# Performance work log

Hardware: AMD Instinct MI355X
Metric: run time of the kernel (lower is better)

## Reference

```python
import jax, jax.numpy as jnp
import numpy as np

# dims from QBN_GRU_Base.__init__ with in_dim=64
IN_DIM = 64
OBS_MID = 28   # int(abs(64 - 8) / 2)
OBS_BN = 8
M_SIZE = 16
LATENT = 16
M_BN = 8
T, B = 512, 2048


def _lin_params(key, out_d, in_d):
    # normc init: normal(0,1) rows scaled to unit L2 norm, zero bias
    w = jax.random.normal(key, (out_d, in_d), dtype=jnp.float32)
    w = w / jnp.sqrt(jnp.sum(w * w, axis=1, keepdims=True))
    b = jnp.zeros((out_d,), dtype=jnp.float32)
    return w, b


def setup_inputs() -> dict:
    key = jax.random.key(0)
    ks = jax.random.split(key, 16)
    x = jax.random.normal(ks[0], (T, B, IN_DIM), dtype=jnp.float32)
    obs_w0, obs_b0 = _lin_params(ks[1], OBS_MID, IN_DIM)
    obs_w1, obs_b1 = _lin_params(ks[2], OBS_MID, OBS_MID)
    obs_w2, obs_b2 = _lin_params(ks[3], OBS_BN, OBS_MID)
    s = float(1.0 / np.sqrt(M_SIZE))  # torch GRUCell default init
    gru_wih = jax.random.uniform(ks[4], (3 * M_SIZE, OBS_BN), jnp.float32, -s, s)
    gru_whh = jax.random.uniform(ks[5], (3 * M_SIZE, M_SIZE), jnp.float32, -s, s)
    gru_bih = jax.random.uniform(ks[6], (3 * M_SIZE,), jnp.float32, -s, s)
    gru_bhh = jax.random.uniform(ks[7], (3 * M_SIZE,), jnp.float32, -s, s)
    m2q_w0, m2q_b0 = _lin_params(ks[8], LATENT, M_SIZE)
    m2q_w1, m2q_b1 = _lin_params(ks[9], LATENT, LATENT)
    m2q_w2, m2q_b2 = _lin_params(ks[10], M_BN, LATENT)
    q2m_w0, q2m_b0 = _lin_params(ks[11], LATENT, M_BN)
    q2m_w1, q2m_b1 = _lin_params(ks[12], LATENT, LATENT)
    q2m_w2, q2m_b2 = _lin_params(ks[13], M_SIZE, LATENT)
    act_w, act_b = _lin_params(ks[14], LATENT, M_SIZE)
    return dict(x=x,
                obs_w0=obs_w0, obs_b0=obs_b0, obs_w1=obs_w1, obs_b1=obs_b1,
                obs_w2=obs_w2, obs_b2=obs_b2,
                gru_wih=gru_wih, gru_whh=gru_whh, gru_bih=gru_bih, gru_bhh=gru_bhh,
                m2q_w0=m2q_w0, m2q_b0=m2q_b0, m2q_w1=m2q_w1, m2q_b1=m2q_b1,
                m2q_w2=m2q_w2, m2q_b2=m2q_b2,
                q2m_w0=q2m_w0, q2m_b0=q2m_b0, q2m_w1=q2m_w1, q2m_b1=q2m_b1,
                q2m_w2=q2m_w2, q2m_b2=q2m_b2,
                act_w=act_w, act_b=act_b)


def _ternary_tanh(v):
    # QBN soft ternary activation with straight-through rounding to {-1,0,1}
    soft = 1.5 * jnp.tanh(v) + 0.5 * jnp.tanh(-3.0 * v)
    return soft + jax.lax.stop_gradient(jnp.round(soft) - soft)


def reference(x, obs_w0, obs_b0, obs_w1, obs_b1, obs_w2, obs_b2,
              gru_wih, gru_whh, gru_bih, gru_bhh,
              m2q_w0, m2q_b0, m2q_w1, m2q_b1, m2q_w2, m2q_b2,
              q2m_w0, q2m_b0, q2m_w1, q2m_b1, q2m_w2, q2m_b2,
              act_w, act_b):
    # observation QBN encoder, applied to all timesteps at once [T,B,in]->[T,B,8]
    h = jnp.tanh(x @ obs_w0.T + obs_b0)
    h = jnp.tanh(h @ obs_w1.T + obs_b1)
    xq = _ternary_tanh(h @ obs_w2.T + obs_b2)

    def step(hid, x_t):
        # torch.nn.GRUCell math
        gi = x_t @ gru_wih.T + gru_bih        # [B, 3*M]
        gh = hid @ gru_whh.T + gru_bhh
        ir, iz, inn = jnp.split(gi, 3, axis=-1)
        hr, hz, hn = jnp.split(gh, 3, axis=-1)
        r = jax.nn.sigmoid(ir + hr)
        z = jax.nn.sigmoid(iz + hz)
        n = jnp.tanh(inn + r * hn)
        ht = (1.0 - z) * n + z * hid
        # memory -> quantized bottleneck
        q = jnp.tanh(ht @ m2q_w0.T + m2q_b0)
        q = jnp.tanh(q @ m2q_w1.T + m2q_b1)
        q = _ternary_tanh(q @ m2q_w2.T + m2q_b2)
        # bottleneck -> memory (all layers tanh)
        m = jnp.tanh(q @ q2m_w0.T + q2m_b0)
        m = jnp.tanh(m @ q2m_w1.T + q2m_b1)
        m = jnp.tanh(m @ q2m_w2.T + q2m_b2)
        return m, m  # new hidden, and per-step output y

    h0 = jnp.zeros((x.shape[1], M_SIZE), dtype=x.dtype)
    _, ys = jax.lax.scan(step, h0, xq)        # [T, B, M_SIZE]
    return jnp.tanh(ys @ act_w.T + act_b)     # action latent [T, B, LATENT]
```

## Files before the change

### kernel.cpp

```cpp
#include <hip/hip_runtime.h>


#define T_DIM 512
#define B_DIM 2048
#define NELEM (T_DIM * B_DIM)

__device__ __forceinline__ float tanh_xla(float x) {
  const float kClamp = 7.99881172180175781f;
  float xc = fminf(fmaxf(x, -kClamp), kClamp);
  float x2 = xc * xc;
  float p = fmaf(x2, -2.76076847742355e-16f, 2.00018790482477e-13f);
  p = fmaf(x2, p, -8.60467152213735e-11f);
  p = fmaf(x2, p, 5.12229709037114e-08f);
  p = fmaf(x2, p, 1.48572235717979e-05f);
  p = fmaf(x2, p, 6.37261928875436e-04f);
  p = fmaf(x2, p, 4.89352455891786e-03f);
  p = xc * p;
  float q = fmaf(x2, 1.19825839466702e-06f, 1.18534705686654e-04f);
  q = fmaf(x2, q, 2.26843463243900e-03f);
  q = fmaf(x2, q, 4.89352518554385e-03f);
  float r = p / q;
  return (fabsf(x) < 0.0004f) ? x : r;
}

__device__ __forceinline__ float sigmoid_xla(float x) {
  return 0.5f + 0.5f * tanh_xla(0.5f * x);
}

__device__ __forceinline__ int ternary_digit(float v) {
  float soft = 1.5f * tanh_xla(v) + 0.5f * tanh_xla(-3.0f * v);
  return (int)rintf(soft) + 1;
}

__global__ __launch_bounds__(256) void k_obs(
    const float* __restrict__ x,
    const float* __restrict__ w0, const float* __restrict__ b0,
    const float* __restrict__ w1, const float* __restrict__ b1,
    const float* __restrict__ w2, const float* __restrict__ b2,
    unsigned short* __restrict__ xcodes) {
  int e = blockIdx.x * 256 + threadIdx.x;
  const float* xr = x + (size_t)e * 64;
  float xv[64];
#pragma unroll
  for (int j = 0; j < 64; j += 4) {
    float4 v = *reinterpret_cast<const float4*>(xr + j);
    xv[j] = v.x; xv[j + 1] = v.y; xv[j + 2] = v.z; xv[j + 3] = v.w;
  }
  float h1[28];
#pragma unroll
  for (int k = 0; k < 28; ++k) {
    float acc = 0.0f;
#pragma unroll
    for (int j = 0; j < 64; ++j) acc = fmaf(w0[k * 64 + j], xv[j], acc);
    h1[k] = tanh_xla(acc + b0[k]);
  }
  float h2[28];
#pragma unroll
  for (int k = 0; k < 28; ++k) {
    float acc = 0.0f;
#pragma unroll
    for (int j = 0; j < 28; ++j) acc = fmaf(w1[k * 28 + j], h1[j], acc);
    h2[k] = tanh_xla(acc + b1[k]);
  }
  const int p3[8] = {1, 3, 9, 27, 81, 243, 729, 2187};
  unsigned code = 0;
#pragma unroll
  for (int k = 0; k < 8; ++k) {
    float acc = 0.0f;
#pragma unroll
    for (int j = 0; j < 28; ++j) acc = fmaf(w2[k * 28 + j], h2[j], acc);
    code += (unsigned)(ternary_digit(acc + b2[k]) * p3[k]);
  }
  xcodes[e] = (unsigned short)code;
}

__global__ __launch_bounds__(256) void k_gi(
    const float* __restrict__ wih, const float* __restrict__ bih,
    float* __restrict__ gip) {
  int c = blockIdx.x * 256 + threadIdx.x;
  if (c >= 6561) return;
  float q[8];
  unsigned cc = (unsigned)c;
#pragma unroll
  for (int k = 0; k < 8; ++k) { q[k] = (float)((int)(cc % 3u) - 1); cc /= 3u; }
#pragma unroll
  for (int i = 0; i < 16; ++i) {
    float gr = 0.f, gz = 0.f, gn = 0.f;
#pragma unroll
    for (int j = 0; j < 8; ++j) {
      gr = fmaf(wih[i * 8 + j], q[j], gr);
      gz = fmaf(wih[(16 + i) * 8 + j], q[j], gz);
      gn = fmaf(wih[(32 + i) * 8 + j], q[j], gn);
    }
    float4 o;
    o.x = gr + bih[i]; o.y = gz + bih[16 + i]; o.z = gn + bih[32 + i]; o.w = 0.f;
    *reinterpret_cast<float4*>(gip + (size_t)c * 64 + i * 4) = o;
  }
}

__global__ __launch_bounds__(256) void k_mtab(
    const float* __restrict__ q2m_w0, const float* __restrict__ q2m_b0,
    const float* __restrict__ q2m_w1, const float* __restrict__ q2m_b1,
    const float* __restrict__ q2m_w2, const float* __restrict__ q2m_b2,
    const float* __restrict__ whh, const float* __restrict__ bhh,
    const float* __restrict__ act_w, const float* __restrict__ act_b,
    float* __restrict__ ghm, float* __restrict__ ytab) {
  int c = blockIdx.x * 256 + threadIdx.x;
  if (c > 6561) return;
  float m[16];
  if (c == 6561) {
#pragma unroll
    for (int i = 0; i < 16; ++i) m[i] = 0.0f;
  } else {
    float q[8];
    unsigned cc = (unsigned)c;
#pragma unroll
    for (int k = 0; k < 8; ++k) { q[k] = (float)((int)(cc % 3u) - 1); cc /= 3u; }
    float a[16];
#pragma unroll
    for (int i = 0; i < 16; ++i) {
      float acc = 0.f;
#pragma unroll
      for (int j = 0; j < 8; ++j) acc = fmaf(q2m_w0[i * 8 + j], q[j], acc);
      a[i] = tanh_xla(acc + q2m_b0[i]);
    }
    float d[16];
#pragma unroll
    for (int i = 0; i < 16; ++i) {
      float acc = 0.f;
#pragma unroll
      for (int j = 0; j < 16; ++j) acc = fmaf(q2m_w1[i * 16 + j], a[j], acc);
      d[i] = tanh_xla(acc + q2m_b1[i]);
    }
#pragma unroll
    for (int i = 0; i < 16; ++i) {
      float acc = 0.f;
#pragma unroll
      for (int j = 0; j < 16; ++j) acc = fmaf(q2m_w2[i * 16 + j], d[j], acc);
      m[i] = tanh_xla(acc + q2m_b2[i]);
    }
  }
#pragma unroll
  for (int i = 0; i < 16; ++i) {
    float gr = 0.f, gz = 0.f, gn = 0.f;
#pragma unroll
    for (int j = 0; j < 16; ++j) {
      gr = fmaf(whh[i * 16 + j], m[j], gr);
      gz = fmaf(whh[(16 + i) * 16 + j], m[j], gz);
      gn = fmaf(whh[(32 + i) * 16 + j], m[j], gn);
    }
    float4 o;
    o.x = gr + bhh[i]; o.y = gz + bhh[16 + i]; o.z = gn + bhh[32 + i]; o.w = m[i];
    *reinterpret_cast<float4*>(ghm + (size_t)c * 64 + i * 4) = o;
  }
  if (c < 6561) {
#pragma unroll
    for (int i = 0; i < 16; ++i) {
      float acc = 0.f;
#pragma unroll
      for (int j = 0; j < 16; ++j) acc = fmaf(act_w[i * 16 + j], m[j], acc);
      ytab[(size_t)c * 16 + i] = tanh_xla(acc + act_b[i]);
    }
  }
}

__global__ __launch_bounds__(64) void k_scan(
    const unsigned short* __restrict__ xcodes,
    const float* __restrict__ ghm,
    const float* __restrict__ gip,
    const float* __restrict__ m2q_w0, const float* __restrict__ m2q_b0,
    const float* __restrict__ m2q_w1, const float* __restrict__ m2q_b1,
    const float* __restrict__ m2q_w2, const float* __restrict__ m2q_b2,
    unsigned short* __restrict__ qcodes) {
  int lane = threadIdx.x & 15;
  int b = (blockIdx.x * 64 + threadIdx.x) >> 4;
  float w0r[16], w1r[16], w2r[16];
#pragma unroll
  for (int j = 0; j < 16; j += 4) {
    float4 a = *reinterpret_cast<const float4*>(m2q_w0 + lane * 16 + j);
    w0r[j] = a.x; w0r[j + 1] = a.y; w0r[j + 2] = a.z; w0r[j + 3] = a.w;
    float4 bq = *reinterpret_cast<const float4*>(m2q_w1 + lane * 16 + j);
    w1r[j] = bq.x; w1r[j + 1] = bq.y; w1r[j + 2] = bq.z; w1r[j + 3] = bq.w;
    float4 cq = *reinterpret_cast<const float4*>(m2q_w2 + (lane & 7) * 16 + j);
    w2r[j] = cq.x; w2r[j + 1] = cq.y; w2r[j + 2] = cq.z; w2r[j + 3] = cq.w;
  }
  float b0l = m2q_b0[lane], b1l = m2q_b1[lane], b2l = m2q_b2[lane & 7];
  const int ip3[8] = {1, 3, 9, 27, 81, 243, 729, 2187};
  int p3 = (lane < 8) ? ip3[lane & 7] : 0;

  unsigned qprev = 6561;
  unsigned xc = xcodes[b];
  float4 i4 = *reinterpret_cast<const float4*>(gip + (size_t)xc * 64 + lane * 4);

  for (int t = 0; t < T_DIM; ++t) {
    float4 g4 = *reinterpret_cast<const float4*>(ghm + (size_t)qprev * 64 + lane * 4);
    int tn = (t + 1 < T_DIM) ? t + 1 : T_DIM - 1;
    unsigned xcn = xcodes[tn * B_DIM + b];
    float4 i4n = *reinterpret_cast<const float4*>(gip + (size_t)xcn * 64 + lane * 4);

    float r = sigmoid_xla(i4.x + g4.x);
    float z = sigmoid_xla(i4.y + g4.y);
    float n = tanh_xla(fmaf(r, g4.z, i4.z));
    float h = (1.0f - z) * n + z * g4.w;

    float acc = 0.f;
#pragma unroll
    for (int j = 0; j < 16; ++j) acc = fmaf(w0r[j], __shfl(h, j, 16), acc);
    float t0 = tanh_xla(acc + b0l);
    acc = 0.f;
#pragma unroll
    for (int j = 0; j < 16; ++j) acc = fmaf(w1r[j], __shfl(t0, j, 16), acc);
    float t1 = tanh_xla(acc + b1l);
    acc = 0.f;
#pragma unroll
    for (int j = 0; j < 16; ++j) acc = fmaf(w2r[j], __shfl(t1, j, 16), acc);
    int val = ternary_digit(acc + b2l) * p3;
    val += __shfl_xor(val, 1, 16);
    val += __shfl_xor(val, 2, 16);
    val += __shfl_xor(val, 4, 16);
    val += __shfl_xor(val, 8, 16);
    qprev = (unsigned)val;
    if (lane == 0) qcodes[t * B_DIM + b] = (unsigned short)qprev;
    xc = xcn;
    i4 = i4n;
  }
}

__global__ __launch_bounds__(256) void k_out(
    const unsigned short* __restrict__ qcodes,
    const float* __restrict__ ytab,
    float* __restrict__ out) {
  int i = blockIdx.x * 256 + threadIdx.x;
  int e = i >> 2, sub = i & 3;
  unsigned c = qcodes[e];
  float4 y = *reinterpret_cast<const float4*>(ytab + (size_t)c * 16 + sub * 4);
  reinterpret_cast<float4*>(out)[i] = y;
}

extern "C" void kernel_launch(void* const* d_in, const int* in_sizes, int n_in,
                              void* d_out, int out_size, void* d_ws, size_t ws_size,
                              hipStream_t stream) {
  (void)in_sizes; (void)n_in; (void)out_size; (void)ws_size;
  const float* x       = (const float*)d_in[0];
  const float* obs_w0  = (const float*)d_in[1];
  const float* obs_b0  = (const float*)d_in[2];
  const float* obs_w1  = (const float*)d_in[3];
  const float* obs_b1  = (const float*)d_in[4];
  const float* obs_w2  = (const float*)d_in[5];
  const float* obs_b2  = (const float*)d_in[6];
  const float* gru_wih = (const float*)d_in[7];
  const float* gru_whh = (const float*)d_in[8];
  const float* gru_bih = (const float*)d_in[9];
  const float* gru_bhh = (const float*)d_in[10];
  const float* m2q_w0  = (const float*)d_in[11];
  const float* m2q_b0  = (const float*)d_in[12];
  const float* m2q_w1  = (const float*)d_in[13];
  const float* m2q_b1  = (const float*)d_in[14];
  const float* m2q_w2  = (const float*)d_in[15];
  const float* m2q_b2  = (const float*)d_in[16];
  const float* q2m_w0  = (const float*)d_in[17];
  const float* q2m_b0  = (const float*)d_in[18];
  const float* q2m_w1  = (const float*)d_in[19];
  const float* q2m_b1  = (const float*)d_in[20];
  const float* q2m_w2  = (const float*)d_in[21];
  const float* q2m_b2  = (const float*)d_in[22];
  const float* act_w   = (const float*)d_in[23];
  const float* act_b   = (const float*)d_in[24];

  char* ws = (char*)d_ws;
  unsigned short* xcodes = (unsigned short*)(ws);
  unsigned short* qcodes = (unsigned short*)(ws + (2u << 20));
  float* gip  = (float*)(ws + (4u << 20));
  float* ghm  = (float*)(ws + (6u << 20));
  float* ytab = (float*)(ws + (8u << 20));

  k_gi<<<26, 256, 0, stream>>>(gru_wih, gru_bih, gip);
  k_mtab<<<26, 256, 0, stream>>>(q2m_w0, q2m_b0, q2m_w1, q2m_b1, q2m_w2, q2m_b2,
                                 gru_whh, gru_bhh, act_w, act_b, ghm, ytab);
  k_obs<<<NELEM / 256, 256, 0, stream>>>(x, obs_w0, obs_b0, obs_w1, obs_b1,
                                         obs_w2, obs_b2, xcodes);
  k_scan<<<(B_DIM * 16) / 64, 64, 0, stream>>>(xcodes, ghm, gip,
                                               m2q_w0, m2q_b0, m2q_w1, m2q_b1,
                                               m2q_w2, m2q_b2, qcodes);
  k_out<<<(NELEM * 4) / 256, 256, 0, stream>>>(qcodes, ytab, (float*)d_out);
}
```

Measured before the change: 1.128 ms.

## Give each batch row its own wavefront and use readlane instead of shuffles

The scan kernel now maps one batch element per 64-thread block (one wavefront) instead of four elements per wavefront. Because the row is wave-uniform, cross-lane broadcasts use scalar readlane instead of ds_bpermute shuffles, and the ternary code is built from eight readlanes rather than a butterfly reduction. This shortens the per-step serial dependency latency but leaves 48 of 64 lanes idle and quadruples the number of wavefronts launched.

```diff
diff --git a/kernel.cpp b/kernel.cpp
--- a/kernel.cpp
+++ b/kernel.cpp
@@ -32,6 +32,10 @@
   return (int)rintf(soft) + 1;
 }
 
+__device__ __forceinline__ float blane(float v, int j) {
+  return __int_as_float(__builtin_amdgcn_readlane(__float_as_int(v), j));
+}
+
 __global__ __launch_bounds__(256) void k_obs(
     const float* __restrict__ x,
     const float* __restrict__ w0, const float* __restrict__ b0,
@@ -172,8 +176,9 @@
     const float* __restrict__ m2q_w1, const float* __restrict__ m2q_b1,
     const float* __restrict__ m2q_w2, const float* __restrict__ m2q_b2,
     unsigned short* __restrict__ qcodes) {
-  int lane = threadIdx.x & 15;
-  int b = (blockIdx.x * 64 + threadIdx.x) >> 4;
+  const int lane = threadIdx.x & 15;
+  const int b = blockIdx.x;
+
   float w0r[16], w1r[16], w2r[16];
 #pragma unroll
   for (int j = 0; j < 16; j += 4) {
@@ -184,19 +189,20 @@
     float4 cq = *reinterpret_cast<const float4*>(m2q_w2 + (lane & 7) * 16 + j);
     w2r[j] = cq.x; w2r[j + 1] = cq.y; w2r[j + 2] = cq.z; w2r[j + 3] = cq.w;
   }
-  float b0l = m2q_b0[lane], b1l = m2q_b1[lane], b2l = m2q_b2[lane & 7];
-  const int ip3[8] = {1, 3, 9, 27, 81, 243, 729, 2187};
-  int p3 = (lane < 8) ? ip3[lane & 7] : 0;
-
-  unsigned qprev = 6561;
+  const float b0l = m2q_b0[lane], b1l = m2q_b1[lane], b2l = m2q_b2[lane & 7];
+
+  const float4* __restrict__ ghm4 = (const float4*)ghm;
+  const float4* __restrict__ gip4 = (const float4*)gip;
+
+  int qcode = 6561;
   unsigned xc = xcodes[b];
-  float4 i4 = *reinterpret_cast<const float4*>(gip + (size_t)xc * 64 + lane * 4);
+  float4 i4 = gip4[(int)xc * 16 + lane];
 
   for (int t = 0; t < T_DIM; ++t) {
-    float4 g4 = *reinterpret_cast<const float4*>(ghm + (size_t)qprev * 64 + lane * 4);
+    float4 g4 = ghm4[qcode * 16 + lane];
     int tn = (t + 1 < T_DIM) ? t + 1 : T_DIM - 1;
     unsigned xcn = xcodes[tn * B_DIM + b];
-    float4 i4n = *reinterpret_cast<const float4*>(gip + (size_t)xcn * 64 + lane * 4);
+    float4 i4n = gip4[(int)xcn * 16 + lane];
 
     float r = sigmoid_xla(i4.x + g4.x);
     float z = sigmoid_xla(i4.y + g4.y);
@@ -205,23 +211,28 @@
 
     float acc = 0.f;
 #pragma unroll
-    for (int j = 0; j < 16; ++j) acc = fmaf(w0r[j], __shfl(h, j, 16), acc);
+    for (int j = 0; j < 16; ++j) acc = fmaf(w0r[j], blane(h, j), acc);
     float t0 = tanh_xla(acc + b0l);
     acc = 0.f;
 #pragma unroll
-    for (int j = 0; j < 16; ++j) acc = fmaf(w1r[j], __shfl(t0, j, 16), acc);
+    for (int j = 0; j < 16; ++j) acc = fmaf(w1r[j], blane(t0, j), acc);
     float t1 = tanh_xla(acc + b1l);
     acc = 0.f;
 #pragma unroll
-    for (int j = 0; j < 16; ++j) acc = fmaf(w2r[j], __shfl(t1, j, 16), acc);
-    int val = ternary_digit(acc + b2l) * p3;
-    val += __shfl_xor(val, 1, 16);
-    val += __shfl_xor(val, 2, 16);
-    val += __shfl_xor(val, 4, 16);
-    val += __shfl_xor(val, 8, 16);
-    qprev = (unsigned)val;
-    if (lane == 0) qcodes[t * B_DIM + b] = (unsigned short)qprev;
-    xc = xcn;
+    for (int j = 0; j < 16; ++j) acc = fmaf(w2r[j], blane(t1, j), acc);
+    int d = ternary_digit(acc + b2l);
+
+    int qc = __builtin_amdgcn_readlane(d, 0);
+    qc += __builtin_amdgcn_readlane(d, 1) * 3;
+    qc += __builtin_amdgcn_readlane(d, 2) * 9;
+    qc += __builtin_amdgcn_readlane(d, 3) * 27;
+    qc += __builtin_amdgcn_readlane(d, 4) * 81;
+    qc += __builtin_amdgcn_readlane(d, 5) * 243;
+    qc += __builtin_amdgcn_readlane(d, 6) * 729;
+    qc += __builtin_amdgcn_readlane(d, 7) * 2187;
+    qcode = qc;
+
+    if (threadIdx.x == 0) qcodes[t * B_DIM + b] = (unsigned short)qcode;
     i4 = i4n;
   }
 }
@@ -279,8 +290,8 @@
                                  gru_whh, gru_bhh, act_w, act_b, ghm, ytab);
   k_obs<<<NELEM / 256, 256, 0, stream>>>(x, obs_w0, obs_b0, obs_w1, obs_b1,
                                          obs_w2, obs_b2, xcodes);
-  k_scan<<<(B_DIM * 16) / 64, 64, 0, stream>>>(xcodes, ghm, gip,
-                                               m2q_w0, m2q_b0, m2q_w1, m2q_b1,
-                                               m2q_w2, m2q_b2, qcodes);
+  k_scan<<<B_DIM, 64, 0, stream>>>(xcodes, ghm, gip,
+                                   m2q_w0, m2q_b0, m2q_w1, m2q_b1,
+                                   m2q_w2, m2q_b2, qcodes);
   k_out<<<(NELEM * 4) / 256, 256, 0, stream>>>(qcodes, ytab, (float*)d_out);
 }
```

New measurement: 1.420 ms. 1.26x slower.
